# Optimization experiments

Measured on AMD Instinct MI355X. Metric: run time of the kernel, lower is better.

## Reference

```python
import jax, jax.numpy as jnp
import numpy as np
import math

MIN_INTEGRAL = 1e-05
INTERVAL_TIME = 0.05


def setup_inputs() -> dict:
    key = jax.random.key(0)
    ks = jax.random.split(key, 8)
    B, S, U, W = 8192, 256, 128, 512  # batch, state, user_params, hidden width
    D_in = S + U
    sc = lambda fan_in: 1.0 / np.sqrt(fan_in)
    return {
        "state": jax.random.normal(ks[0], (B, S), dtype=jnp.float32),
        "user_params": jax.random.normal(ks[1], (B, U), dtype=jnp.float32),
        "W1": jax.random.normal(ks[2], (D_in, W), dtype=jnp.float32) * sc(D_in),
        "b1": jax.random.normal(ks[3], (W,), dtype=jnp.float32) * 0.01,
        "W2": jax.random.normal(ks[4], (W, W), dtype=jnp.float32) * sc(W),
        "b2": jax.random.normal(ks[5], (W,), dtype=jnp.float32) * 0.01,
        "W3": jax.random.normal(ks[6], (W, S), dtype=jnp.float32) * sc(W),
        "b3": jax.random.normal(ks[7], (S,), dtype=jnp.float32) * 0.01,
        "h": 1,
    }


def reference(state, user_params, W1, b1, W2, b2, W3, b3, h):
    # ode_func: cat(state, user_params) -> Linear -> SiLU -> Linear -> SiLU -> Linear
    def ode_func(s):
        x = jnp.concatenate((s, user_params), axis=1)
        x = jax.nn.silu(x @ W1 + b1)
        x = jax.nn.silu(x @ W2 + b2)
        return x @ W3 + b3

    num_intervals = int(math.floor(h / INTERVAL_TIME))  # fp-faithful to torch code

    def step(s, _):
        return s + ode_func(s) * INTERVAL_TIME, None

    state, _ = jax.lax.scan(step, state, None, length=num_intervals)

    rest_interval = h % INTERVAL_TIME
    if MIN_INTEGRAL < rest_interval:
        # NOTE: original code adds the derivative WITHOUT scaling by rest_interval
        state = state + ode_func(state)
    return state
```

## Files before the change

kernel.cpp:

```cpp
#include <hip/hip_runtime.h>

typedef __attribute__((ext_vector_type(8))) short short8;
typedef __attribute__((ext_vector_type(4))) float float4v;
typedef unsigned short u16;

#define Sdim 256
#define Udim 128
#define Hdim 512
#define MT   32
#define XS   392
#define XLS  264
#define HS   520
#define NW   589824
#define W1_OFF 0
#define W2_OFF 196608
#define W3_OFF 458752
#define NSTEPS 21

__device__ __forceinline__ float bf2f(u16 u) {
    union { unsigned int i; float f; } x; x.i = ((unsigned int)u) << 16; return x.f;
}
__device__ __forceinline__ u16 f2bf(float f) {
    union { float f; unsigned int i; } x; x.f = f;
    unsigned int r = x.i + 0x7FFFu + ((x.i >> 16) & 1u);
    return (u16)(r >> 16);
}

__device__ __forceinline__ int probe_local(const u16* __restrict__ w1, int tid) {
    __shared__ int cnt;
    if (tid == 0) cnt = 0;
    __syncthreads();
    if (tid < 256) {
        u16 u = w1[tid];
        int e = (u >> 7) & 0xFF;
        if ((u == 0) || (e >= 0x60 && e <= 0x8F)) atomicAdd(&cnt, 1);
    }
    __syncthreads();
    return (cnt >= 240) ? 1 : 0;
}

template<int KT, int N>
__device__ __forceinline__ void pack_one(const void* __restrict__ Wraw,
                                         u16* __restrict__ hi, int e, int bf) {
    int f = e >> 3, j = e & 7;
    int lane = f & 63, tile = f >> 6;
    int kt = tile % KT, nt = tile / KT;
    int k = kt * 32 + ((lane >> 4) << 3) + j;
    int n = nt * 16 + (lane & 15);
    float wv = bf ? bf2f(((const u16*)Wraw)[(size_t)k * N + n])
                  : ((const float*)Wraw)[(size_t)k * N + n];
    hi[e] = f2bf(wv);
}

__global__ void pack_all(const void* __restrict__ W1, const void* __restrict__ W2,
                         const void* __restrict__ W3, u16* __restrict__ wh,
                         int* __restrict__ flagp) {
    int bf = probe_local((const u16*)W1, threadIdx.x);
    int g = blockIdx.x * 256 + threadIdx.x;
    if (g == 0) *flagp = bf;
    if (g < W2_OFF)
        pack_one<12, 512>(W1, wh + W1_OFF, g - W1_OFF, bf);
    else if (g < W3_OFF)
        pack_one<16, 512>(W2, wh + W2_OFF, g - W2_OFF, bf);
    else
        pack_one<16, 256>(W3, wh + W3_OFF, g - W3_OFF, bf);
}

#define MFMA __builtin_amdgcn_mfma_f32_16x16x32_bf16

template<int KT0, int KT, int KTB, int KTL, int NT>
__device__ __forceinline__ void mm1(const u16* ah, const u16* al, const int as, const int als,
                                    const u16* __restrict__ wh, float4v acc[2][NT]) {
#pragma unroll 2
    for (int kt = KT0; kt < KT; ++kt) {
        short8 A0 = *(const short8*)(ah + kt * 32);
        short8 A1 = *(const short8*)(ah + 16 * as + kt * 32);
        short8 A0l, A1l;
        if (kt < KTL) {
            A0l = *(const short8*)(al + kt * 32);
            A1l = *(const short8*)(al + 16 * als + kt * 32);
        }
#pragma unroll
        for (int t = 0; t < NT; ++t) {
            short8 Bh = *(const short8*)(wh + (size_t)(t * KTB + kt) * 512);
            acc[0][t] = MFMA(A0, Bh, acc[0][t], 0, 0, 0);
            acc[1][t] = MFMA(A1, Bh, acc[1][t], 0, 0, 0);
            if (kt < KTL) {
                acc[0][t] = MFMA(A0l, Bh, acc[0][t], 0, 0, 0);
                acc[1][t] = MFMA(A1l, Bh, acc[1][t], 0, 0, 0);
            }
        }
    }
}

__device__ __forceinline__ float silu(float v) {
    return v * __builtin_amdgcn_rcpf(1.0f + __expf(-v));
}

template<bool BF>
__device__ __forceinline__ void body(
    const void* state_raw, const void* user_raw,
    const void* b1r, const void* b2r, const void* b3r,
    const u16* __restrict__ wh_all, void* outp,
    u16* xh, u16* xl, u16* H1, u16* H2) {

    const int tid = threadIdx.x, w = tid >> 6, lane = tid & 63;
    const int col16 = lane & 15, quad = lane >> 4;
    const int r0 = blockIdx.x * MT;

    if (tid < 512) {
        int row = tid >> 4;
        int c8 = (tid & 15) * 8;
        if (BF) {
            short8 v = *(const short8*)((const u16*)user_raw + (size_t)(r0 + row) * Udim + c8);
            *(short8*)(xh + row * XS + Sdim + c8) = v;
        } else {
            const float* up = (const float*)user_raw + (size_t)(r0 + row) * Udim + c8;
            short8 v;
#pragma unroll
            for (int j = 0; j < 8; ++j) v[j] = (short)f2bf(up[j]);
            *(short8*)(xh + row * XS + Sdim + c8) = v;
        }
    }
    float b1f[2], b2f[2], b3f;
#pragma unroll
    for (int t = 0; t < 2; ++t) {
        int i = w * 32 + t * 16 + col16;
        b1f[t] = BF ? bf2f(((const u16*)b1r)[i]) : ((const float*)b1r)[i];
        b2f[t] = BF ? bf2f(((const u16*)b2r)[i]) : ((const float*)b2r)[i];
    }
    {
        int i = w * 16 + col16;
        b3f = BF ? bf2f(((const u16*)b3r)[i]) : ((const float*)b3r)[i];
    }
    float st[2][4];
#pragma unroll
    for (int m = 0; m < 2; ++m)
#pragma unroll
        for (int r = 0; r < 4; ++r) {
            int row = m * 16 + quad * 4 + r;
            int col = w * 16 + col16;
            float v = BF ? bf2f(((const u16*)state_raw)[(size_t)(r0 + row) * Sdim + col])
                         : ((const float*)state_raw)[(size_t)(r0 + row) * Sdim + col];
            st[m][r] = v;
            u16 h = f2bf(v);
            xh[row * XS + col] = h;
            xl[row * XLS + col] = f2bf(v - bf2f(h));
        }
    __syncthreads();

    const u16* w1h = wh_all + W1_OFF + (size_t)(w * 2) * 12 * 512 + lane * 8;
    const u16* w2h = wh_all + W2_OFF + (size_t)(w * 2) * 16 * 512 + lane * 8;
    const u16* w3h = wh_all + W3_OFF + (size_t)(w)     * 16 * 512 + lane * 8;

    const u16* aXh = xh + col16 * XS + quad * 8;
    const u16* aXl = xl + col16 * XLS + quad * 8;
    const u16* aH1 = H1 + col16 * HS + quad * 8;
    const u16* aH2 = H2 + col16 * HS + quad * 8;

    float4v uacc[2][2];
#pragma unroll
    for (int m = 0; m < 2; ++m)
#pragma unroll
        for (int t = 0; t < 2; ++t) uacc[m][t] = (float4v){b1f[t], b1f[t], b1f[t], b1f[t]};
    mm1<8, 12, 12, 0, 2>(aXh, aXh, XS, XS, w1h, uacc);

    for (int step = 0; step < NSTEPS; ++step) {
        const float dt = (step == NSTEPS - 1) ? 1.0f : 0.05f;
        const bool lo_now = (step == 0) || (step == NSTEPS - 1);

        {
            float4v acc[2][2];
#pragma unroll
            for (int m = 0; m < 2; ++m)
#pragma unroll
                for (int t = 0; t < 2; ++t) acc[m][t] = uacc[m][t];
            if (lo_now) mm1<0, 8, 12, 8, 2>(aXh, aXl, XS, XLS, w1h, acc);
            else        mm1<0, 8, 12, 0, 2>(aXh, aXl, XS, XLS, w1h, acc);
#pragma unroll
            for (int m = 0; m < 2; ++m)
#pragma unroll
                for (int t = 0; t < 2; ++t)
#pragma unroll
                    for (int r = 0; r < 4; ++r) {
                        float s = silu(acc[m][t][r]);
                        H1[(m * 16 + quad * 4 + r) * HS + w * 32 + t * 16 + col16] = f2bf(s);
                    }
        }
        __syncthreads();

        {
            float4v acc[2][2];
#pragma unroll
            for (int m = 0; m < 2; ++m)
#pragma unroll
                for (int t = 0; t < 2; ++t) acc[m][t] = (float4v){b2f[t], b2f[t], b2f[t], b2f[t]};
            mm1<0, 16, 16, 0, 2>(aH1, aH1, HS, HS, w2h, acc);
#pragma unroll
            for (int m = 0; m < 2; ++m)
#pragma unroll
                for (int t = 0; t < 2; ++t)
#pragma unroll
                    for (int r = 0; r < 4; ++r) {
                        float s = silu(acc[m][t][r]);
                        H2[(m * 16 + quad * 4 + r) * HS + w * 32 + t * 16 + col16] = f2bf(s);
                    }
        }
        __syncthreads();

        {
            float4v acc[2][1];
#pragma unroll
            for (int m = 0; m < 2; ++m) acc[m][0] = (float4v){b3f, b3f, b3f, b3f};
            mm1<0, 16, 16, 0, 1>(aH2, aH2, HS, HS, w3h, acc);
#pragma unroll
            for (int m = 0; m < 2; ++m)
#pragma unroll
                for (int r = 0; r < 4; ++r) {
                    float v = st[m][r] + acc[m][0][r] * dt;
                    st[m][r] = v;
                    if (step < NSTEPS - 1) {
                        int row = m * 16 + quad * 4 + r;
                        int col = w * 16 + col16;
                        u16 h = f2bf(v);
                        xh[row * XS + col] = h;
                        if (step == NSTEPS - 2)
                            xl[row * XLS + col] = f2bf(v - bf2f(h));
                    }
                }
        }
        __syncthreads();
    }

#pragma unroll
    for (int m = 0; m < 2; ++m)
#pragma unroll
        for (int r = 0; r < 4; ++r) {
            int row = m * 16 + quad * 4 + r;
            int col = w * 16 + col16;
            if (BF) ((u16*)outp)[(size_t)(r0 + row) * Sdim + col] = f2bf(st[m][r]);
            else    ((float*)outp)[(size_t)(r0 + row) * Sdim + col] = st[m][r];
        }
}

__global__ __launch_bounds__(1024, 4) void fused_ode(
    const void* state_raw, const void* user_raw,
    const void* b1r, const void* b2r, const void* b3r,
    const u16* __restrict__ wh, const int* __restrict__ flagp, void* outp) {

    __shared__ __align__(16) u16 xh[MT * XS];
    __shared__ __align__(16) u16 xl[MT * XLS];
    __shared__ __align__(16) u16 H1[MT * HS];
    __shared__ __align__(16) u16 H2[MT * HS];

    if (*flagp)
        body<true >(state_raw, user_raw, b1r, b2r, b3r, wh, outp, xh, xl, H1, H2);
    else
        body<false>(state_raw, user_raw, b1r, b2r, b3r, wh, outp, xh, xl, H1, H2);
}

extern "C" void kernel_launch(void* const* d_in, const int* in_sizes, int n_in,
                              void* d_out, int out_size, void* d_ws, size_t ws_size,
                              hipStream_t stream) {
    u16* wh = (u16*)d_ws;
    int* flagp = (int*)((char*)d_ws + (size_t)NW * sizeof(u16));

    pack_all<<<NW / 256, 256, 0, stream>>>(d_in[2], d_in[4], d_in[6], wh, flagp);

    fused_ode<<<8192 / MT, 1024, 0, stream>>>(d_in[0], d_in[1], d_in[3], d_in[5], d_in[7],
                                              wh, flagp, d_out);
}
```

Before: 318.5 us.

## Propagate layer-1 preactivation via precomputed W3·W1[:S] product instead of recomputing

Since layer 1 is linear in state, the kernel keeps its preactivation z in registers and updates it with z += dt·(H2·G + b3·W1s), where G = W3·W1[:S] is precomputed in bf16 by a new pack kernel. This removes the per-step layer-1 GEMM over the state part (K=256) and the writes of state into shared memory. In exchange, the layer-3 pass now also computes a 512-wide G product, which adds MFMA work. It also changes numerics, because G is rounded to bf16 and the hi/lo split precision on state is lost after the first step.

```diff
diff --git a/kernel.cpp b/kernel.cpp
--- a/kernel.cpp
+++ b/kernel.cpp
@@ -1,6 +1,7 @@
 #include <hip/hip_runtime.h>
 
 typedef __attribute__((ext_vector_type(8))) short short8;
+typedef __attribute__((ext_vector_type(4))) short short4v;
 typedef __attribute__((ext_vector_type(4))) float float4v;
 typedef unsigned short u16;
 
@@ -15,6 +16,9 @@
 #define W1_OFF 0
 #define W2_OFF 196608
 #define W3_OFF 458752
+#define G_OFF  589824
+#define C3_OFF 851968
+#define FLAG_BYTE 1705984
 #define NSTEPS 21
 
 __device__ __forceinline__ float bf2f(u16 u) {
@@ -68,6 +72,76 @@
 
 #define MFMA __builtin_amdgcn_mfma_f32_16x16x32_bf16
 
+__global__ void pack_G(const void* __restrict__ W3raw, const void* __restrict__ W1raw,
+                       u16* __restrict__ wh, const int* __restrict__ flagp) {
+    const int bf = *flagp;
+    const int lane = threadIdx.x;
+    const int col16 = lane & 15, quad = lane >> 4;
+    const int bi = blockIdx.x & 15;
+    const int bj = blockIdx.x >> 4;
+    float4v acc[2][2];
+#pragma unroll
+    for (int m = 0; m < 2; ++m)
+#pragma unroll
+        for (int t = 0; t < 2; ++t) acc[m][t] = (float4v){0.f, 0.f, 0.f, 0.f};
+#pragma unroll 2
+    for (int kt = 0; kt < 8; ++kt) {
+        const int k0 = kt * 32 + quad * 8;
+        short8 A0, A1, B0, B1;
+#pragma unroll
+        for (int j = 0; j < 8; ++j) {
+            const int kk = k0 + j;
+            const int ra0 = bi * 32 + col16, ra1 = ra0 + 16;
+            const int cb0 = bj * 32 + col16, cb1 = cb0 + 16;
+            float a0, a1, b0, b1;
+            if (bf) {
+                a0 = bf2f(((const u16*)W3raw)[(size_t)ra0 * 256 + kk]);
+                a1 = bf2f(((const u16*)W3raw)[(size_t)ra1 * 256 + kk]);
+                b0 = bf2f(((const u16*)W1raw)[(size_t)kk * 512 + cb0]);
+                b1 = bf2f(((const u16*)W1raw)[(size_t)kk * 512 + cb1]);
+            } else {
+                a0 = ((const float*)W3raw)[(size_t)ra0 * 256 + kk];
+                a1 = ((const float*)W3raw)[(size_t)ra1 * 256 + kk];
+                b0 = ((const float*)W1raw)[(size_t)kk * 512 + cb0];
+                b1 = ((const float*)W1raw)[(size_t)kk * 512 + cb1];
+            }
+            A0[j] = (short)f2bf(a0); A1[j] = (short)f2bf(a1);
+            B0[j] = (short)f2bf(b0); B1[j] = (short)f2bf(b1);
+        }
+        acc[0][0] = MFMA(A0, B0, acc[0][0], 0, 0, 0);
+        acc[0][1] = MFMA(A0, B1, acc[0][1], 0, 0, 0);
+        acc[1][0] = MFMA(A1, B0, acc[1][0], 0, 0, 0);
+        acc[1][1] = MFMA(A1, B1, acc[1][1], 0, 0, 0);
+    }
+#pragma unroll
+    for (int m = 0; m < 2; ++m)
+#pragma unroll
+        for (int t = 0; t < 2; ++t) {
+            short4v pv;
+#pragma unroll
+            for (int r = 0; r < 4; ++r) pv[r] = (short)f2bf(acc[m][t][r]);
+            const int ntp = bj * 2 + t;
+            const int lanep = col16 + 16 * (m * 2 + (quad >> 1));
+            u16* dst = wh + G_OFF + ((size_t)(ntp * 16 + bi)) * 512 + lanep * 8 + (quad & 1) * 4;
+            *reinterpret_cast<short4v*>(dst) = pv;
+        }
+}
+
+__global__ void pack_c3(const void* __restrict__ b3r, const void* __restrict__ W1raw,
+                        float* __restrict__ c3, const int* __restrict__ flagp) {
+    const int bf = *flagp;
+    const int j = blockIdx.x * 128 + threadIdx.x;
+    float s = 0.f;
+#pragma unroll 4
+    for (int k = 0; k < 256; ++k) {
+        float b = bf ? bf2f(((const u16*)b3r)[k]) : ((const float*)b3r)[k];
+        float wv = bf ? bf2f(((const u16*)W1raw)[(size_t)k * 512 + j])
+                      : ((const float*)W1raw)[(size_t)k * 512 + j];
+        s += b * wv;
+    }
+    c3[j] = s;
+}
+
 template<int KT0, int KT, int KTB, int KTL, int NT>
 __device__ __forceinline__ void mm1(const u16* ah, const u16* al, const int as, const int als,
                                     const u16* __restrict__ wh, float4v acc[2][NT]) {
@@ -93,6 +167,25 @@
     }
 }
 
+__device__ __forceinline__ void mmA(const u16* ah, const int as,
+                                    const u16* __restrict__ w3, const u16* __restrict__ g,
+                                    float4v facc[2][1], float4v gacc[2][2]) {
+#pragma unroll 2
+    for (int kt = 0; kt < 16; ++kt) {
+        short8 A0 = *(const short8*)(ah + kt * 32);
+        short8 A1 = *(const short8*)(ah + 16 * as + kt * 32);
+        short8 Bw = *(const short8*)(w3 + (size_t)kt * 512);
+        facc[0][0] = MFMA(A0, Bw, facc[0][0], 0, 0, 0);
+        facc[1][0] = MFMA(A1, Bw, facc[1][0], 0, 0, 0);
+#pragma unroll
+        for (int t = 0; t < 2; ++t) {
+            short8 Bg = *(const short8*)(g + (size_t)(t * 16 + kt) * 512);
+            gacc[0][t] = MFMA(A0, Bg, gacc[0][t], 0, 0, 0);
+            gacc[1][t] = MFMA(A1, Bg, gacc[1][t], 0, 0, 0);
+        }
+    }
+}
+
 __device__ __forceinline__ float silu(float v) {
     return v * __builtin_amdgcn_rcpf(1.0f + __expf(-v));
 }
@@ -101,7 +194,7 @@
 __device__ __forceinline__ void body(
     const void* state_raw, const void* user_raw,
     const void* b1r, const void* b2r, const void* b3r,
-    const u16* __restrict__ wh_all, void* outp,
+    const u16* __restrict__ wh_all, const float* __restrict__ c3p, void* outp,
     u16* xh, u16* xl, u16* H1, u16* H2) {
 
     const int tid = threadIdx.x, w = tid >> 6, lane = tid & 63;
@@ -122,12 +215,13 @@
             *(short8*)(xh + row * XS + Sdim + c8) = v;
         }
     }
-    float b1f[2], b2f[2], b3f;
+    float b1f[2], b2f[2], b3f, c3f[2];
 #pragma unroll
     for (int t = 0; t < 2; ++t) {
         int i = w * 32 + t * 16 + col16;
         b1f[t] = BF ? bf2f(((const u16*)b1r)[i]) : ((const float*)b1r)[i];
         b2f[t] = BF ? bf2f(((const u16*)b2r)[i]) : ((const float*)b2r)[i];
+        c3f[t] = c3p[i];
     }
     {
         int i = w * 16 + col16;
@@ -152,6 +246,7 @@
     const u16* w1h = wh_all + W1_OFF + (size_t)(w * 2) * 12 * 512 + lane * 8;
     const u16* w2h = wh_all + W2_OFF + (size_t)(w * 2) * 16 * 512 + lane * 8;
     const u16* w3h = wh_all + W3_OFF + (size_t)(w)     * 16 * 512 + lane * 8;
+    const u16* gh  = wh_all + G_OFF  + (size_t)(w * 2) * 16 * 512 + lane * 8;
 
     const u16* aXh = xh + col16 * XS + quad * 8;
     const u16* aXl = xl + col16 * XLS + quad * 8;
@@ -165,35 +260,29 @@
         for (int t = 0; t < 2; ++t) uacc[m][t] = (float4v){b1f[t], b1f[t], b1f[t], b1f[t]};
     mm1<8, 12, 12, 0, 2>(aXh, aXh, XS, XS, w1h, uacc);
 
-    for (int step = 0; step < NSTEPS; ++step) {
-        const float dt = (step == NSTEPS - 1) ? 1.0f : 0.05f;
-        const bool lo_now = (step == 0) || (step == NSTEPS - 1);
-
+    float4v z[2][2];
+#pragma unroll
+    for (int m = 0; m < 2; ++m)
+#pragma unroll
+        for (int t = 0; t < 2; ++t) z[m][t] = (float4v){0.f, 0.f, 0.f, 0.f};
+    mm1<0, 8, 12, 8, 2>(aXh, aXl, XS, XLS, w1h, z);
+
+#pragma unroll
+    for (int m = 0; m < 2; ++m)
+#pragma unroll
+        for (int t = 0; t < 2; ++t)
+#pragma unroll
+            for (int r = 0; r < 4; ++r)
+                H1[(m * 16 + quad * 4 + r) * HS + w * 32 + t * 16 + col16] =
+                    f2bf(silu(z[m][t][r] + uacc[m][t][r]));
+    __syncthreads();
+
+    for (int s = 0; s < NSTEPS; ++s) {
         {
             float4v acc[2][2];
 #pragma unroll
             for (int m = 0; m < 2; ++m)
 #pragma unroll
-                for (int t = 0; t < 2; ++t) acc[m][t] = uacc[m][t];
-            if (lo_now) mm1<0, 8, 12, 8, 2>(aXh, aXl, XS, XLS, w1h, acc);
-            else        mm1<0, 8, 12, 0, 2>(aXh, aXl, XS, XLS, w1h, acc);
-#pragma unroll
-            for (int m = 0; m < 2; ++m)
-#pragma unroll
-                for (int t = 0; t < 2; ++t)
-#pragma unroll
-                    for (int r = 0; r < 4; ++r) {
-                        float s = silu(acc[m][t][r]);
-                        H1[(m * 16 + quad * 4 + r) * HS + w * 32 + t * 16 + col16] = f2bf(s);
-                    }
-        }
-        __syncthreads();
-
-        {
-            float4v acc[2][2];
-#pragma unroll
-            for (int m = 0; m < 2; ++m)
-#pragma unroll
                 for (int t = 0; t < 2; ++t) acc[m][t] = (float4v){b2f[t], b2f[t], b2f[t], b2f[t]};
             mm1<0, 16, 16, 0, 2>(aH1, aH1, HS, HS, w2h, acc);
 #pragma unroll
@@ -201,33 +290,44 @@
 #pragma unroll
                 for (int t = 0; t < 2; ++t)
 #pragma unroll
+                    for (int r = 0; r < 4; ++r)
+                        H2[(m * 16 + quad * 4 + r) * HS + w * 32 + t * 16 + col16] =
+                            f2bf(silu(acc[m][t][r]));
+        }
+        __syncthreads();
+
+        if (s < NSTEPS - 1) {
+            float4v facc[2][1], gacc[2][2];
+#pragma unroll
+            for (int m = 0; m < 2; ++m) {
+                facc[m][0] = (float4v){b3f, b3f, b3f, b3f};
+#pragma unroll
+                for (int t = 0; t < 2; ++t) gacc[m][t] = (float4v){0.f, 0.f, 0.f, 0.f};
+            }
+            mmA(aH2, HS, w3h, gh, facc, gacc);
+#pragma unroll
+            for (int m = 0; m < 2; ++m) {
+#pragma unroll
+                for (int t = 0; t < 2; ++t)
+#pragma unroll
                     for (int r = 0; r < 4; ++r) {
-                        float s = silu(acc[m][t][r]);
-                        H2[(m * 16 + quad * 4 + r) * HS + w * 32 + t * 16 + col16] = f2bf(s);
+                        float zv = z[m][t][r] + 0.05f * (gacc[m][t][r] + c3f[t]);
+                        z[m][t][r] = zv;
+                        H1[(m * 16 + quad * 4 + r) * HS + w * 32 + t * 16 + col16] =
+                            f2bf(silu(zv + uacc[m][t][r]));
                     }
-        }
-        __syncthreads();
-
-        {
-            float4v acc[2][1];
-#pragma unroll
-            for (int m = 0; m < 2; ++m) acc[m][0] = (float4v){b3f, b3f, b3f, b3f};
-            mm1<0, 16, 16, 0, 1>(aH2, aH2, HS, HS, w3h, acc);
+#pragma unroll
+                for (int r = 0; r < 4; ++r) st[m][r] += 0.05f * facc[m][0][r];
+            }
+        } else {
+            float4v facc[2][1];
+#pragma unroll
+            for (int m = 0; m < 2; ++m) facc[m][0] = (float4v){b3f, b3f, b3f, b3f};
+            mm1<0, 16, 16, 0, 1>(aH2, aH2, HS, HS, w3h, facc);
 #pragma unroll
             for (int m = 0; m < 2; ++m)
 #pragma unroll
-                for (int r = 0; r < 4; ++r) {
-                    float v = st[m][r] + acc[m][0][r] * dt;
-                    st[m][r] = v;
-                    if (step < NSTEPS - 1) {
-                        int row = m * 16 + quad * 4 + r;
-                        int col = w * 16 + col16;
-                        u16 h = f2bf(v);
-                        xh[row * XS + col] = h;
-                        if (step == NSTEPS - 2)
-                            xl[row * XLS + col] = f2bf(v - bf2f(h));
-                    }
-                }
+                for (int r = 0; r < 4; ++r) st[m][r] += facc[m][0][r];
         }
         __syncthreads();
     }
@@ -246,7 +346,8 @@
 __global__ __launch_bounds__(1024, 4) void fused_ode(
     const void* state_raw, const void* user_raw,
     const void* b1r, const void* b2r, const void* b3r,
-    const u16* __restrict__ wh, const int* __restrict__ flagp, void* outp) {
+    const u16* __restrict__ wh, const float* __restrict__ c3p,
+    const int* __restrict__ flagp, void* outp) {
 
     __shared__ __align__(16) u16 xh[MT * XS];
     __shared__ __align__(16) u16 xl[MT * XLS];
@@ -254,19 +355,22 @@
     __shared__ __align__(16) u16 H2[MT * HS];
 
     if (*flagp)
-        body<true >(state_raw, user_raw, b1r, b2r, b3r, wh, outp, xh, xl, H1, H2);
+        body<true >(state_raw, user_raw, b1r, b2r, b3r, wh, c3p, outp, xh, xl, H1, H2);
     else
-        body<false>(state_raw, user_raw, b1r, b2r, b3r, wh, outp, xh, xl, H1, H2);
+        body<false>(state_raw, user_raw, b1r, b2r, b3r, wh, c3p, outp, xh, xl, H1, H2);
 }
 
 extern "C" void kernel_launch(void* const* d_in, const int* in_sizes, int n_in,
                               void* d_out, int out_size, void* d_ws, size_t ws_size,
                               hipStream_t stream) {
     u16* wh = (u16*)d_ws;
-    int* flagp = (int*)((char*)d_ws + (size_t)NW * sizeof(u16));
+    float* c3 = (float*)(wh + C3_OFF);
+    int* flagp = (int*)((char*)d_ws + FLAG_BYTE);
 
     pack_all<<<NW / 256, 256, 0, stream>>>(d_in[2], d_in[4], d_in[6], wh, flagp);
+    pack_G<<<256, 64, 0, stream>>>(d_in[6], d_in[2], wh, flagp);
+    pack_c3<<<4, 128, 0, stream>>>(d_in[7], d_in[2], c3, flagp);
 
     fused_ode<<<8192 / MT, 1024, 0, stream>>>(d_in[0], d_in[1], d_in[3], d_in[5], d_in[7],
-                                              wh, flagp, d_out);
-}
+                                              wh, c3, flagp, d_out);
+}
```

Result: slower. 401.5 us (+26.1%).
